# Performance work log

Hardware: AMD Instinct MI355X
Metric: run time of the kernel (lower is better)

## Reference

```python
import jax, jax.numpy as jnp
import numpy as np

KP, KD = 25, 3          # keypoints_num, keypoint_dim
FEAT = KP * KD          # 75
H = 1024                # hidden_size
NOISE_VALUE = 0.0
HT_LIMIT = 1.0


def lstm_cell(x, h, c, Wih, Whh, bih, bhh):
    # PyTorch LSTMCell gate order: i, f, g, o
    gates = x @ Wih.T + bih + h @ Whh.T + bhh  # [B, 4H]
    i, f, g, o = jnp.split(gates, 4, axis=-1)
    c = jax.nn.sigmoid(f) * c + jax.nn.sigmoid(i) * jnp.tanh(g)
    h = jax.nn.sigmoid(o) * jnp.tanh(c)
    return h, c


def run_lstm(seq, Wih, Whh, bih, bhh):
    # seq: [T, B, F]; single-layer LSTM, zero init state. Returns final (h, c).
    B = seq.shape[1]
    h0 = jnp.zeros((B, Whh.shape[1]), seq.dtype)
    def step(carry, x):
        h, c = lstm_cell(x, carry[0], carry[1], Wih, Whh, bih, bhh)
        return (h, c), None
    (h, c), _ = jax.lax.scan(step, (h0, h0), seq)
    return h, c


def setup_inputs() -> dict:
    key = jax.random.key(0)
    ks = jax.random.split(key, 20)
    s = 0.02
    inp = {
        'observed_pose': jax.random.normal(ks[0], (1024, 50, FEAT), jnp.float32),
        'future_pose': jax.random.normal(ks[1], (1024, 25, FEAT), jnp.float32),
        'observed_noise': jax.random.randint(ks[2], (1024, 50, KP), 0, 2, jnp.int32),
        # pose encoder LSTM params
        'pe_Wih': jax.random.normal(ks[3], (4 * H, FEAT), jnp.float32) * s,
        'pe_Whh': jax.random.normal(ks[4], (4 * H, H), jnp.float32) * s,
        'pe_bih': jax.random.normal(ks[5], (4 * H,), jnp.float32) * s,
        'pe_bhh': jax.random.normal(ks[6], (4 * H,), jnp.float32) * s,
        # vel encoder LSTM params
        've_Wih': jax.random.normal(ks[7], (4 * H, FEAT), jnp.float32) * s,
        've_Whh': jax.random.normal(ks[8], (4 * H, H), jnp.float32) * s,
        've_bih': jax.random.normal(ks[9], (4 * H,), jnp.float32) * s,
        've_bhh': jax.random.normal(ks[10], (4 * H,), jnp.float32) * s,
        # decoder LSTMCell params
        'dec_Wih': jax.random.normal(ks[11], (4 * H, FEAT), jnp.float32) * s,
        'dec_Whh': jax.random.normal(ks[12], (4 * H, H), jnp.float32) * s,
        'dec_bih': jax.random.normal(ks[13], (4 * H,), jnp.float32) * s,
        'dec_bhh': jax.random.normal(ks[14], (4 * H,), jnp.float32) * s,
        # output projection
        'fc_W': jax.random.normal(ks[15], (FEAT, H), jnp.float32) * s,
        'fc_b': jax.random.normal(ks[16], (FEAT,), jnp.float32) * s,
    }
    return inp


def reference(observed_pose, future_pose, observed_noise,
              pe_Wih, pe_Whh, pe_bih, pe_bhh,
              ve_Wih, ve_Whh, ve_bih, ve_bhh,
              dec_Wih, dec_Whh, dec_bih, dec_bhh,
              fc_W, fc_b):
    pose = observed_pose                              # [B, T, FEAT]
    vel = pose[:, 1:, :] - pose[:, :-1, :]            # [B, T-1, FEAT]
    bs, fn, feat = vel.shape
    noise = observed_noise[:, 1:, :]                  # [B, T-1, KP]
    mask = (noise == 1)[..., None]                    # [B, T-1, KP, 1]
    vel = jnp.where(mask, jnp.float32(NOISE_VALUE),
                    vel.reshape(bs, fn, KP, KD)).reshape(bs, fn, feat)

    h_vel, c_vel = run_lstm(vel.transpose(1, 0, 2), ve_Wih, ve_Whh, ve_bih, ve_bhh)
    h_pose, c_pose = run_lstm(pose.transpose(1, 0, 2), pe_Wih, pe_Whh, pe_bih, pe_bhh)

    h = h_pose + h_vel
    c = c_pose + c_vel
    out0 = vel[:, -1, :]                              # decoder seed input

    def dec_step(carry, _):
        h, c, out = carry
        x = jax.lax.stop_gradient(out)                # .detach() in the original
        h, c = lstm_cell(x, h, c, dec_Wih, dec_Whh, dec_bih, dec_bhh)
        out = jnp.clip(h @ fc_W.T + fc_b, -HT_LIMIT, HT_LIMIT)  # Hardtanh
        return (h, c, out), out

    _, comp_vel = jax.lax.scan(dec_step, (h, c, out0), None, length=fn)
    comp_vel = comp_vel.transpose(1, 0, 2)            # [B, T-1, FEAT]

    # comp_pose[0] = pose[0]; comp_pose[i+1] = comp_pose[i] + comp_vel[i]
    comp_pose = jnp.concatenate(
        [pose[:, :1], pose[:, :1] + jnp.cumsum(comp_vel, axis=1)], axis=1)

    return future_pose, comp_pose, comp_vel
```

## Files before the change

### kernel.cpp

```cpp
#include <hip/hip_runtime.h>

typedef unsigned short ushort_t;
typedef __attribute__((ext_vector_type(8))) short bf16x8;
typedef __attribute__((ext_vector_type(4))) float f32x4;

#define B_    1024
#define H_    1024
#define FEAT_ 75
#define KP_   1120
#define NK_   35
#define OFF_CP 1920000UL
#define OFF_CV 5760000UL

__device__ __forceinline__ float bf2f(ushort_t u) {
    unsigned x = ((unsigned)u) << 16;
    float f; __builtin_memcpy(&f, &x, 4); return f;
}
__device__ __forceinline__ ushort_t f2bf(float f) {
    unsigned x; __builtin_memcpy(&x, &f, 4);
    x += 0x7fffu + ((x >> 16) & 1u);
    return (ushort_t)(x >> 16);
}
__device__ __forceinline__ float sigm(float x) { return 1.f / (1.f + __expf(-x)); }

__device__ __forceinline__ void gload16(const void* g, void* l) {
    __builtin_amdgcn_global_load_lds(
        (const __attribute__((address_space(1))) void*)g,
        (__attribute__((address_space(3))) void*)l, 16, 0, 0);
}

struct StepArgs {
    const ushort_t* Ain[2];
    ushort_t*       Aout[2];
    const ushort_t* W[2];
    const float*    bias[2];
    float*          c[2];
    const ushort_t* xnext[2];
    int             xstride[2];
};

__global__ __launch_bounds__(256)
void lstm_step_kernel(StepArgs sa)
{
    __shared__ __align__(16) char lds[2 * 20480];

    const int flat = blockIdx.x;
    const int xcd  = flat & 7;
    const int slot = flat >> 3;
    int p, ct, rt;
    if (gridDim.x == 512) {
        const int cg = (xcd << 2) + (slot >> 4);
        p  = cg >> 4;
        ct = cg & 15;
    } else {
        const int cg = (xcd << 1) + (slot >> 4);
        p  = 0;
        ct = cg;
    }
    rt = slot & 15;

    const ushort_t* __restrict__ Ain  = sa.Ain[p];
    ushort_t*       __restrict__ Aout = sa.Aout[p];
    const ushort_t* __restrict__ Wt   = sa.W[p];
    const float*    __restrict__ bias = sa.bias[p];
    float*          __restrict__ cst  = sa.c[p];
    const ushort_t* xnext = sa.xnext[p];
    const int xstride = sa.xstride[p];

    const int tid  = threadIdx.x;
    const int w    = tid >> 6;
    const int l    = tid & 63;
    const int j0   = ct * 64;
    const int row0 = rt * 64;

    if (ct == 0 && xnext) {
        for (int idx = tid; idx < 64 * 96; idx += 256) {
            const int r  = idx / 96;
            const int xi = idx - r * 96;
            const int grow = row0 + r;
            ushort_t v = (xi < FEAT_) ? xnext[(size_t)grow * xstride + xi] : (ushort_t)0;
            Aout[(size_t)grow * KP_ + 1024 + xi] = v;
        }
    }

    const int lc4  = l & 3;
    const int lr4  = l >> 2;
    const int csrc = lc4 ^ (lr4 & 3);

    const ushort_t* agsrc = Ain + (size_t)(row0 + w * 16 + lr4) * KP_ + csrc * 8;
    char* aldst = lds + (w * 16) * 64;

    const ushort_t* bgsrc[4];
    char* bldst[4];
    #pragma unroll
    for (int i = 0; i < 4; ++i) {
        const int wcol = w * 1024 + j0 + i * 16 + lr4;
        bgsrc[i] = Wt + (size_t)wcol * KP_ + csrc * 8;
        bldst[i] = lds + 4096 + (w * 64 + i * 16) * 64;
    }

    const int chsw = (((l >> 4) ^ (l & 3)) << 4);
    int aoff[4], boff[4];
    #pragma unroll
    for (int m = 0; m < 4; ++m) aoff[m] = (m * 16 + (l & 15)) * 64 + chsw;
    #pragma unroll
    for (int g = 0; g < 4; ++g) boff[g] = 4096 + (g * 64 + w * 16 + (l & 15)) * 64 + chsw;

    f32x4 acc[4][4];
    #pragma unroll
    for (int m = 0; m < 4; ++m)
        #pragma unroll
        for (int g = 0; g < 4; ++g)
            acc[m][g] = (f32x4){0.f, 0.f, 0.f, 0.f};

    gload16(agsrc, aldst);
    #pragma unroll
    for (int i = 0; i < 4; ++i) gload16(bgsrc[i], bldst[i]);

    int bi = 0;
    for (int kt = 0; kt < NK_; ++kt) {
        if (kt + 1 < NK_) {
            const size_t k0 = (size_t)(kt + 1) * 32;
            const int nb = (bi ^ 1) * 20480;
            gload16(agsrc + k0, aldst + nb);
            #pragma unroll
            for (int i = 0; i < 4; ++i) gload16(bgsrc[i] + k0, bldst[i] + nb);
            asm volatile("s_waitcnt vmcnt(5)" ::: "memory");
        } else {
            asm volatile("s_waitcnt vmcnt(0)" ::: "memory");
        }
        __builtin_amdgcn_s_barrier();
        asm volatile("" ::: "memory");

        const char* bp = lds + bi * 20480;
        bf16x8 a[4], b[4];
        #pragma unroll
        for (int m = 0; m < 4; ++m) a[m] = *(const bf16x8*)(bp + aoff[m]);
        #pragma unroll
        for (int g = 0; g < 4; ++g) b[g] = *(const bf16x8*)(bp + boff[g]);
        __builtin_amdgcn_s_setprio(1);
        #pragma unroll
        for (int m = 0; m < 4; ++m)
            #pragma unroll
            for (int g = 0; g < 4; ++g)
                acc[m][g] = __builtin_amdgcn_mfma_f32_16x16x32_bf16(a[m], b[g], acc[m][g], 0, 0, 0);
        __builtin_amdgcn_s_setprio(0);

        asm volatile("" ::: "memory");
        __builtin_amdgcn_s_barrier();
        bi ^= 1;
    }

    const int jw = j0 + w * 16 + (l & 15);
    const float b_i = bias[jw];
    const float b_f = bias[1024 + jw];
    const float b_g = bias[2048 + jw];
    const float b_o = bias[3072 + jw];
    #pragma unroll
    for (int m = 0; m < 4; ++m) {
        #pragma unroll
        for (int r = 0; r < 4; ++r) {
            const int grow = row0 + m * 16 + ((l >> 4) << 2) + r;
            const float gi = acc[m][0][r] + b_i;
            const float gf = acc[m][1][r] + b_f;
            const float gg = acc[m][2][r] + b_g;
            const float go = acc[m][3][r] + b_o;
            const size_t ce = (size_t)grow * H_ + jw;
            const float cn = sigm(gf) * cst[ce] + sigm(gi) * tanhf(gg);
            cst[ce] = cn;
            Aout[(size_t)grow * KP_ + jw] = f2bf(sigm(go) * tanhf(cn));
        }
    }
}

__global__ __launch_bounds__(256)
void pack_kernel(const float* __restrict__ peWih, const float* __restrict__ peWhh,
                 const float* __restrict__ veWih, const float* __restrict__ veWhh,
                 const float* __restrict__ deWih, const float* __restrict__ deWhh,
                 const float* __restrict__ pe_bih, const float* __restrict__ pe_bhh,
                 const float* __restrict__ ve_bih, const float* __restrict__ ve_bhh,
                 const float* __restrict__ de_bih, const float* __restrict__ de_bhh,
                 const float* __restrict__ fcW,
                 ushort_t* __restrict__ Wp, float* __restrict__ biasp,
                 ushort_t* __restrict__ fcWb)
{
    const size_t PER = 4096UL * KP_;
    const size_t NW  = 3UL * PER;
    const size_t NB  = 3UL * 4096;
    const size_t NF  = 75UL * 1024;
    for (size_t idx = (size_t)blockIdx.x * blockDim.x + threadIdx.x;
         idx < NW + NB + NF; idx += (size_t)gridDim.x * blockDim.x) {
        if (idx < NW) {
            const int p   = (int)(idx / PER);
            const size_t rem = idx % PER;
            const int row = (int)(rem / KP_);
            const int k   = (int)(rem % KP_);
            const float* Whh = (p == 0) ? peWhh : (p == 1) ? veWhh : deWhh;
            const float* Wih = (p == 0) ? peWih : (p == 1) ? veWih : deWih;
            float v = 0.f;
            if (k < 1024)      v = Whh[(size_t)row * 1024 + k];
            else if (k < 1099) v = Wih[(size_t)row * 75 + (k - 1024)];
            Wp[idx] = f2bf(v);
        } else if (idx < NW + NB) {
            const size_t i = idx - NW;
            const int p = (int)(i / 4096);
            const int r = (int)(i % 4096);
            const float* bih = (p == 0) ? pe_bih : (p == 1) ? ve_bih : de_bih;
            const float* bhh = (p == 0) ? pe_bhh : (p == 1) ? ve_bhh : de_bhh;
            biasp[i] = bih[r] + bhh[r];
        } else {
            const size_t i = idx - NW - NB;
            fcWb[i] = f2bf(fcW[i]);
        }
    }
}

__global__ __launch_bounds__(256)
void prep_kernel(const float* __restrict__ pose, const float* __restrict__ fut,
                 const int* __restrict__ noise,
                 ushort_t* __restrict__ pose_bf, ushort_t* __restrict__ vel_bf,
                 ushort_t* __restrict__ A_pe0, ushort_t* __restrict__ A_ve0,
                 ushort_t* __restrict__ A_dec0,
                 float* __restrict__ accp, float* __restrict__ out)
{
    const size_t N0 = 1024UL * 50 * 75;
    const size_t N1 = 1024UL * 49 * 75;
    const size_t N2 = 1920000UL;
    const size_t N3 = 76800UL;
    for (size_t idx = (size_t)blockIdx.x * blockDim.x + threadIdx.x;
         idx < N0 + N1 + N2 + N3; idx += (size_t)gridDim.x * blockDim.x) {
        if (idx < N0) {
            pose_bf[idx] = f2bf(pose[idx]);
        } else if (idx < N0 + N1) {
            const size_t i = idx - N0;
            const int f = (int)(i % 75);
            const size_t rem = i / 75;
            const int t = (int)(rem % 49);
            const size_t b = rem / 49;
            float v = pose[(b * 50 + t + 1) * 75 + f] - pose[(b * 50 + t) * 75 + f];
            if (noise[(b * 50 + t + 1) * 25 + f / 3] == 1) v = 0.f;
            const ushort_t vb = f2bf(v);
            vel_bf[i] = vb;
            if (t == 0)  A_ve0[b * KP_ + 1024 + f]  = vb;
            if (t == 48) A_dec0[b * KP_ + 1024 + f] = vb;
        } else if (idx < N0 + N1 + N2) {
            const size_t i = idx - N0 - N1;
            out[i] = fut[i];
        } else {
            const size_t i = idx - N0 - N1 - N2;
            const size_t b = i / 75;
            const int f = (int)(i % 75);
            const float p0 = pose[b * 50 * 75 + f];
            A_pe0[b * KP_ + 1024 + f] = f2bf(p0);
            accp[i] = p0;
            out[OFF_CP + b * 50 * 75 + f] = p0;
        }
    }
}

__global__ __launch_bounds__(256)
void combine_kernel(const ushort_t* __restrict__ hpe, const ushort_t* __restrict__ hve,
                    const float* __restrict__ cpe, const float* __restrict__ cve,
                    ushort_t* __restrict__ Adec0, float* __restrict__ cde)
{
    const int idx = blockIdx.x * blockDim.x + threadIdx.x;
    if (idx >= B_ * H_) return;
    const int b = idx >> 10, j = idx & 1023;
    Adec0[(size_t)b * KP_ + j] = f2bf(bf2f(hpe[(size_t)b * KP_ + j]) + bf2f(hve[(size_t)b * KP_ + j]));
    cde[idx] = cpe[idx] + cve[idx];
}

__global__ __launch_bounds__(128)
void fc_kernel(const ushort_t* __restrict__ Adec,
               ushort_t* __restrict__ Adec_w,
               const ushort_t* __restrict__ fcWb, const float* __restrict__ fcb,
               float* __restrict__ accp, float* __restrict__ out, int t)
{
    __shared__ float hs[1024];
    const int b = blockIdx.x;
    const ushort_t* hrow = Adec + (size_t)b * KP_;
    {
        const int k = threadIdx.x * 8;
        const bf16x8 v = *(const bf16x8*)(hrow + k);
        #pragma unroll
        for (int u = 0; u < 8; ++u) hs[k + u] = bf2f((ushort_t)v[u]);
    }
    __syncthreads();
    const int f = threadIdx.x;
    if (f < FEAT_) {
        const ushort_t* wr = fcWb + (size_t)f * 1024;
        float s0 = fcb[f], s1 = 0.f, s2 = 0.f, s3 = 0.f;
        for (int k = 0; k < 1024; k += 32) {
            const bf16x8 w0 = *(const bf16x8*)(wr + k);
            const bf16x8 w1 = *(const bf16x8*)(wr + k + 8);
            const bf16x8 w2 = *(const bf16x8*)(wr + k + 16);
            const bf16x8 w3 = *(const bf16x8*)(wr + k + 24);
            #pragma unroll
            for (int u = 0; u < 8; ++u) {
                s0 = fmaf(hs[k + u],      bf2f((ushort_t)w0[u]), s0);
                s1 = fmaf(hs[k + 8 + u],  bf2f((ushort_t)w1[u]), s1);
                s2 = fmaf(hs[k + 16 + u], bf2f((ushort_t)w2[u]), s2);
                s3 = fmaf(hs[k + 24 + u], bf2f((ushort_t)w3[u]), s3);
            }
        }
        float s = (s0 + s1) + (s2 + s3);
        s = fminf(fmaxf(s, -1.f), 1.f);
        const float p = accp[b * FEAT_ + f] + s;
        accp[b * FEAT_ + f] = p;
        out[OFF_CV + ((size_t)b * 49 + t) * FEAT_ + f]     = s;
        out[OFF_CP + ((size_t)b * 50 + t + 1) * FEAT_ + f] = p;
        Adec_w[(size_t)b * KP_ + 1024 + f] = f2bf(s);
    }
}

extern "C" void kernel_launch(void* const* d_in, const int* in_sizes, int n_in,
                              void* d_out, int out_size, void* d_ws, size_t ws_size,
                              hipStream_t stream) {
    const float* pose   = (const float*)d_in[0];
    const float* fut    = (const float*)d_in[1];
    const int*   noise  = (const int*)  d_in[2];
    const float* peWih  = (const float*)d_in[3];
    const float* peWhh  = (const float*)d_in[4];
    const float* pe_bih = (const float*)d_in[5];
    const float* pe_bhh = (const float*)d_in[6];
    const float* veWih  = (const float*)d_in[7];
    const float* veWhh  = (const float*)d_in[8];
    const float* ve_bih = (const float*)d_in[9];
    const float* ve_bhh = (const float*)d_in[10];
    const float* deWih  = (const float*)d_in[11];
    const float* deWhh  = (const float*)d_in[12];
    const float* de_bih = (const float*)d_in[13];
    const float* de_bhh = (const float*)d_in[14];
    const float* fcW    = (const float*)d_in[15];
    const float* fcb    = (const float*)d_in[16];
    float* out = (float*)d_out;

    char* base = (char*)d_ws;
    ushort_t* Ape[2]  = {(ushort_t*)(base + 0UL * 2293760), (ushort_t*)(base + 1UL * 2293760)};
    ushort_t* Ave[2]  = {(ushort_t*)(base + 2UL * 2293760), (ushort_t*)(base + 3UL * 2293760)};
    ushort_t* Adec[2] = {(ushort_t*)(base + 4UL * 2293760), (ushort_t*)(base + 5UL * 2293760)};
    float* c_pe = (float*)(base + 13762560);
    float* c_ve = c_pe + 1048576;
    float* c_de = c_ve + 1048576;
    ushort_t* Wp    = (ushort_t*)(base + 26345472);
    float*    biasp = (float*)   (base + 53870592);
    ushort_t* fcWb  = (ushort_t*)(base + 53919744);
    ushort_t* pose_bf = (ushort_t*)(base + 54073344);
    ushort_t* vel_bf  = (ushort_t*)(base + 61753344);
    float*    accp    = (float*)   (base + 69279744);

    hipMemsetAsync(base, 0, 22151168, stream);

    pack_kernel<<<2048, 256, 0, stream>>>(peWih, peWhh, veWih, veWhh, deWih, deWhh,
                                          pe_bih, pe_bhh, ve_bih, ve_bhh, de_bih, de_bhh,
                                          fcW, Wp, biasp, fcWb);
    prep_kernel<<<2048, 256, 0, stream>>>(pose, fut, noise, pose_bf, vel_bf,
                                          Ape[0], Ave[0], Adec[0], accp, out);

    const ushort_t* Wpe = Wp;
    const ushort_t* Wve = Wp + 4587520;
    const ushort_t* Wde = Wp + 9175040;

    for (int t = 0; t < 49; ++t) {
        StepArgs sa;
        sa.Ain[0] = Ape[t & 1];  sa.Aout[0] = Ape[(t + 1) & 1];
        sa.W[0] = Wpe; sa.bias[0] = biasp; sa.c[0] = c_pe;
        sa.xnext[0] = pose_bf + (size_t)(t + 1) * 75; sa.xstride[0] = 3750;
        sa.Ain[1] = Ave[t & 1];  sa.Aout[1] = Ave[(t + 1) & 1];
        sa.W[1] = Wve; sa.bias[1] = biasp + 4096; sa.c[1] = c_ve;
        sa.xnext[1] = (t < 48) ? (vel_bf + (size_t)(t + 1) * 75) : nullptr;
        sa.xstride[1] = 3675;
        lstm_step_kernel<<<512, 256, 0, stream>>>(sa);
    }
    {
        StepArgs sa;
        sa.Ain[0] = Ape[1]; sa.Aout[0] = Ape[0];
        sa.W[0] = Wpe; sa.bias[0] = biasp; sa.c[0] = c_pe;
        sa.xnext[0] = nullptr; sa.xstride[0] = 3750;
        sa.Ain[1] = sa.Ain[0]; sa.Aout[1] = sa.Aout[0];
        sa.W[1] = sa.W[0]; sa.bias[1] = sa.bias[0]; sa.c[1] = sa.c[0];
        sa.xnext[1] = nullptr; sa.xstride[1] = 3750;
        lstm_step_kernel<<<256, 256, 0, stream>>>(sa);
    }

    combine_kernel<<<4096, 256, 0, stream>>>(Ape[0], Ave[1], c_pe, c_ve, Adec[0], c_de);

    for (int d = 0; d < 49; ++d) {
        StepArgs sa;
        sa.Ain[0] = Adec[d & 1]; sa.Aout[0] = Adec[(d + 1) & 1];
        sa.W[0] = Wde; sa.bias[0] = biasp + 8192; sa.c[0] = c_de;
        sa.xnext[0] = nullptr; sa.xstride[0] = 0;
        sa.Ain[1] = sa.Ain[0]; sa.Aout[1] = sa.Aout[0];
        sa.W[1] = sa.W[0]; sa.bias[1] = sa.bias[0]; sa.c[1] = sa.c[0];
        sa.xnext[1] = nullptr; sa.xstride[1] = 0;
        lstm_step_kernel<<<256, 256, 0, stream>>>(sa);
        fc_kernel<<<B_, 128, 0, stream>>>(Adec[(d + 1) & 1], Adec[(d + 1) & 1],
                                          fcWb, fcb, accp, out, d);
    }
}
```

Before: 4.061 ms.

## Halve LSTM step row tile to 32 and rotate K-loop start per block

Each LSTM step block now covers 32 batch rows instead of 64, which doubles the grid (1024 blocks for the fused encoder pair, 512 for single LSTMs) and trims per-block LDS so that four blocks can fit per CU. Each block starts its K loop at a different offset so that concurrent blocks do not all read the same weight columns at the same time. This aims to fill the GPU better and spread memory traffic across channels, but each weight tile is now loaded by twice as many blocks, roughly doubling weight reads from L2.

```diff
diff --git a/kernel.cpp b/kernel.cpp
--- a/kernel.cpp
+++ b/kernel.cpp
@@ -9,6 +9,7 @@
 #define FEAT_ 75
 #define KP_   1120
 #define NK_   35
+#define LBUF  18432
 #define OFF_CP 1920000UL
 #define OFF_CV 5760000UL
 
@@ -29,52 +30,22 @@
         (__attribute__((address_space(3))) void*)l, 16, 0, 0);
 }
 
-struct StepArgs {
-    const ushort_t* Ain[2];
-    ushort_t*       Aout[2];
-    const ushort_t* W[2];
-    const float*    bias[2];
-    float*          c[2];
-    const ushort_t* xnext[2];
-    int             xstride[2];
-};
-
-__global__ __launch_bounds__(256)
-void lstm_step_kernel(StepArgs sa)
-{
-    __shared__ __align__(16) char lds[2 * 20480];
-
-    const int flat = blockIdx.x;
-    const int xcd  = flat & 7;
-    const int slot = flat >> 3;
-    int p, ct, rt;
-    if (gridDim.x == 512) {
-        const int cg = (xcd << 2) + (slot >> 4);
-        p  = cg >> 4;
-        ct = cg & 15;
-    } else {
-        const int cg = (xcd << 1) + (slot >> 4);
-        p  = 0;
-        ct = cg;
-    }
-    rt = slot & 15;
-
-    const ushort_t* __restrict__ Ain  = sa.Ain[p];
-    ushort_t*       __restrict__ Aout = sa.Aout[p];
-    const ushort_t* __restrict__ Wt   = sa.W[p];
-    const float*    __restrict__ bias = sa.bias[p];
-    float*          __restrict__ cst  = sa.c[p];
-    const ushort_t* xnext = sa.xnext[p];
-    const int xstride = sa.xstride[p];
-
-    const int tid  = threadIdx.x;
+__device__ __forceinline__ void lstm_step_body(
+    char* lds,
+    const ushort_t* __restrict__ Ain, ushort_t* __restrict__ Aout,
+    const ushort_t* __restrict__ Wt,  const float* __restrict__ bias,
+    float* __restrict__ cst,
+    const ushort_t* xnext, int xstride,
+    int ct, int rt, int tid)
+{
     const int w    = tid >> 6;
     const int l    = tid & 63;
     const int j0   = ct * 64;
-    const int row0 = rt * 64;
+    const int row0 = rt * 32;
+    const int rot  = rt >= NK_ ? rt - NK_ : rt;
 
     if (ct == 0 && xnext) {
-        for (int idx = tid; idx < 64 * 96; idx += 256) {
+        for (int idx = tid; idx < 32 * 96; idx += 256) {
             const int r  = idx / 96;
             const int xi = idx - r * 96;
             const int grow = row0 + r;
@@ -82,13 +53,14 @@
             Aout[(size_t)grow * KP_ + 1024 + xi] = v;
         }
     }
+    asm volatile("s_waitcnt vmcnt(0)" ::: "memory");
 
     const int lc4  = l & 3;
     const int lr4  = l >> 2;
     const int csrc = lc4 ^ (lr4 & 3);
 
-    const ushort_t* agsrc = Ain + (size_t)(row0 + w * 16 + lr4) * KP_ + csrc * 8;
-    char* aldst = lds + (w * 16) * 64;
+    const ushort_t* agsrc = Ain + (size_t)(row0 + w * 8 + lr4) * KP_ + csrc * 8;
+    char* aldst = lds + (w * 8) * 64;
 
     const ushort_t* bgsrc[4];
     char* bldst[4];
@@ -96,35 +68,39 @@
     for (int i = 0; i < 4; ++i) {
         const int wcol = w * 1024 + j0 + i * 16 + lr4;
         bgsrc[i] = Wt + (size_t)wcol * KP_ + csrc * 8;
-        bldst[i] = lds + 4096 + (w * 64 + i * 16) * 64;
+        bldst[i] = lds + 2048 + (w * 64 + i * 16) * 64;
     }
 
     const int chsw = (((l >> 4) ^ (l & 3)) << 4);
-    int aoff[4], boff[4];
+    int aoff[2], boff[4];
     #pragma unroll
-    for (int m = 0; m < 4; ++m) aoff[m] = (m * 16 + (l & 15)) * 64 + chsw;
+    for (int m = 0; m < 2; ++m) aoff[m] = (m * 16 + (l & 15)) * 64 + chsw;
     #pragma unroll
-    for (int g = 0; g < 4; ++g) boff[g] = 4096 + (g * 64 + w * 16 + (l & 15)) * 64 + chsw;
-
-    f32x4 acc[4][4];
+    for (int g = 0; g < 4; ++g) boff[g] = 2048 + (g * 64 + w * 16 + (l & 15)) * 64 + chsw;
+
+    f32x4 acc[2][4];
     #pragma unroll
-    for (int m = 0; m < 4; ++m)
+    for (int m = 0; m < 2; ++m)
         #pragma unroll
         for (int g = 0; g < 4; ++g)
             acc[m][g] = (f32x4){0.f, 0.f, 0.f, 0.f};
 
-    gload16(agsrc, aldst);
-    #pragma unroll
-    for (int i = 0; i < 4; ++i) gload16(bgsrc[i], bldst[i]);
+    {
+        const size_t k0 = (size_t)rot * 32;
+        if (l < 32) gload16(agsrc + k0, aldst);
+        #pragma unroll
+        for (int i = 0; i < 4; ++i) gload16(bgsrc[i] + k0, bldst[i]);
+    }
 
     int bi = 0;
-    for (int kt = 0; kt < NK_; ++kt) {
-        if (kt + 1 < NK_) {
-            const size_t k0 = (size_t)(kt + 1) * 32;
-            const int nb = (bi ^ 1) * 20480;
-            gload16(agsrc + k0, aldst + nb);
+    for (int i = 0; i < NK_; ++i) {
+        if (i + 1 < NK_) {
+            int kn = i + 1 + rot; if (kn >= NK_) kn -= NK_;
+            const size_t k0 = (size_t)kn * 32;
+            const int nb = (bi ^ 1) * LBUF;
+            if (l < 32) gload16(agsrc + k0, aldst + nb);
             #pragma unroll
-            for (int i = 0; i < 4; ++i) gload16(bgsrc[i] + k0, bldst[i] + nb);
+            for (int g = 0; g < 4; ++g) gload16(bgsrc[g] + k0, bldst[g] + nb);
             asm volatile("s_waitcnt vmcnt(5)" ::: "memory");
         } else {
             asm volatile("s_waitcnt vmcnt(0)" ::: "memory");
@@ -132,15 +108,15 @@
         __builtin_amdgcn_s_barrier();
         asm volatile("" ::: "memory");
 
-        const char* bp = lds + bi * 20480;
-        bf16x8 a[4], b[4];
-        #pragma unroll
-        for (int m = 0; m < 4; ++m) a[m] = *(const bf16x8*)(bp + aoff[m]);
+        const char* bp = lds + bi * LBUF;
+        bf16x8 a[2], b[4];
+        #pragma unroll
+        for (int m = 0; m < 2; ++m) a[m] = *(const bf16x8*)(bp + aoff[m]);
         #pragma unroll
         for (int g = 0; g < 4; ++g) b[g] = *(const bf16x8*)(bp + boff[g]);
         __builtin_amdgcn_s_setprio(1);
         #pragma unroll
-        for (int m = 0; m < 4; ++m)
+        for (int m = 0; m < 2; ++m)
             #pragma unroll
             for (int g = 0; g < 4; ++g)
                 acc[m][g] = __builtin_amdgcn_mfma_f32_16x16x32_bf16(a[m], b[g], acc[m][g], 0, 0, 0);
@@ -157,7 +133,7 @@
     const float b_g = bias[2048 + jw];
     const float b_o = bias[3072 + jw];
     #pragma unroll
-    for (int m = 0; m < 4; ++m) {
+    for (int m = 0; m < 2; ++m) {
         #pragma unroll
         for (int r = 0; r < 4; ++r) {
             const int grow = row0 + m * 16 + ((l >> 4) << 2) + r;
@@ -171,6 +147,37 @@
             Aout[(size_t)grow * KP_ + jw] = f2bf(sigm(go) * tanhf(cn));
         }
     }
+}
+
+struct StepArgs {
+    const ushort_t* Ain[2];
+    ushort_t*       Aout[2];
+    const ushort_t* W[2];
+    const float*    bias[2];
+    float*          c[2];
+    const ushort_t* xnext[2];
+    int             xstride[2];
+};
+
+__global__ __launch_bounds__(256, 4)
+void step_kernel(StepArgs sa)
+{
+    __shared__ __align__(16) char lds[2 * LBUF];
+    const int flat = blockIdx.x;
+    const int xcd  = flat & 7;
+    const int slot = flat >> 3;
+    int p, ct;
+    if (gridDim.x == 1024) {
+        const int cgx = (xcd << 2) + (slot >> 5);
+        p  = cgx >> 4;
+        ct = cgx & 15;
+    } else {
+        p  = 0;
+        ct = (xcd << 1) + (slot >> 5);
+    }
+    const int rt = slot & 31;
+    lstm_step_body(lds, sa.Ain[p], sa.Aout[p], sa.W[p], sa.bias[p], sa.c[p],
+                   sa.xnext[p], sa.xstride[p], ct, rt, threadIdx.x);
 }
 
 __global__ __launch_bounds__(256)
@@ -266,7 +273,8 @@
     const int idx = blockIdx.x * blockDim.x + threadIdx.x;
     if (idx >= B_ * H_) return;
     const int b = idx >> 10, j = idx & 1023;
-    Adec0[(size_t)b * KP_ + j] = f2bf(bf2f(hpe[(size_t)b * KP_ + j]) + bf2f(hve[(size_t)b * KP_ + j]));
+    const size_t o = (size_t)b * KP_ + j;
+    Adec0[o] = f2bf(bf2f(hpe[o]) + bf2f(hve[o]));
     cde[idx] = cpe[idx] + cve[idx];
 }
 
@@ -370,7 +378,7 @@
         sa.W[1] = Wve; sa.bias[1] = biasp + 4096; sa.c[1] = c_ve;
         sa.xnext[1] = (t < 48) ? (vel_bf + (size_t)(t + 1) * 75) : nullptr;
         sa.xstride[1] = 3675;
-        lstm_step_kernel<<<512, 256, 0, stream>>>(sa);
+        step_kernel<<<1024, 256, 0, stream>>>(sa);
     }
     {
         StepArgs sa;
@@ -380,7 +388,7 @@
         sa.Ain[1] = sa.Ain[0]; sa.Aout[1] = sa.Aout[0];
         sa.W[1] = sa.W[0]; sa.bias[1] = sa.bias[0]; sa.c[1] = sa.c[0];
         sa.xnext[1] = nullptr; sa.xstride[1] = 3750;
-        lstm_step_kernel<<<256, 256, 0, stream>>>(sa);
+        step_kernel<<<512, 256, 0, stream>>>(sa);
     }
 
     combine_kernel<<<4096, 256, 0, stream>>>(Ape[0], Ave[1], c_pe, c_ve, Adec[0], c_de);
@@ -393,7 +401,7 @@
         sa.Ain[1] = sa.Ain[0]; sa.Aout[1] = sa.Aout[0];
         sa.W[1] = sa.W[0]; sa.bias[1] = sa.bias[0]; sa.c[1] = sa.c[0];
         sa.xnext[1] = nullptr; sa.xstride[1] = 0;
-        lstm_step_kernel<<<256, 256, 0, stream>>>(sa);
+        step_kernel<<<512, 256, 0, stream>>>(sa);
         fc_kernel<<<B_, 128, 0, stream>>>(Adec[(d + 1) & 1], Adec[(d + 1) & 1],
                                           fcWb, fcb, accp, out, d);
     }
```

Result: slower. 4.819 ms (+18.7%).

## Fuse all LSTM steps into a persistent cooperative kernel with register-resident weights

Applied to the files above, without the earlier changes.

Replaces roughly 150 per-step kernel launches with one cooperative persistent kernel that uses grid.sync between timesteps. Each wave keeps its slice of the recurrent weight matrix in registers for the whole sequence, and the cell state stays in registers, so per-step weight and state traffic from global memory goes away. The combine and FC projection phases move into the same kernel. The old multi-launch path is kept as a fallback if the cooperative launch fails. In exchange the kernel depends on grid-wide barriers, heavy register pressure (35 bf16x8 per thread at 512 threads with 2 blocks per CU) and only 256 blocks, and the FC phase is scalar.

```diff
diff --git a/kernel.cpp b/kernel.cpp
--- a/kernel.cpp
+++ b/kernel.cpp
@@ -1,4 +1,7 @@
 #include <hip/hip_runtime.h>
+#include <hip/hip_cooperative_groups.h>
+
+namespace cg = cooperative_groups;
 
 typedef unsigned short ushort_t;
 typedef __attribute__((ext_vector_type(8))) short bf16x8;
@@ -8,9 +11,13 @@
 #define H_    1024
 #define FEAT_ 75
 #define KP_   1120
-#define NK_   35
+#define NKT   35
 #define OFF_CP 1920000UL
 #define OFF_CV 5760000UL
+
+#define LDS_SCR 24576
+#define LDS_FC  33280
+#define LDS_TOT 49664
 
 __device__ __forceinline__ float bf2f(ushort_t u) {
     unsigned x = ((unsigned)u) << 16;
@@ -29,147 +36,232 @@
         (__attribute__((address_space(3))) void*)l, 16, 0, 0);
 }
 
-struct StepArgs {
-    const ushort_t* Ain[2];
-    ushort_t*       Aout[2];
-    const ushort_t* W[2];
-    const float*    bias[2];
-    float*          c[2];
-    const ushort_t* xnext[2];
-    int             xstride[2];
-};
-
-__global__ __launch_bounds__(256)
-void lstm_step_kernel(StepArgs sa)
-{
-    __shared__ __align__(16) char lds[2 * 20480];
-
-    const int flat = blockIdx.x;
-    const int xcd  = flat & 7;
-    const int slot = flat >> 3;
-    int p, ct, rt;
-    if (gridDim.x == 512) {
-        const int cg = (xcd << 2) + (slot >> 4);
-        p  = cg >> 4;
-        ct = cg & 15;
-    } else {
-        const int cg = (xcd << 1) + (slot >> 4);
-        p  = 0;
-        ct = cg;
-    }
-    rt = slot & 15;
-
-    const ushort_t* __restrict__ Ain  = sa.Ain[p];
-    ushort_t*       __restrict__ Aout = sa.Aout[p];
-    const ushort_t* __restrict__ Wt   = sa.W[p];
-    const float*    __restrict__ bias = sa.bias[p];
-    float*          __restrict__ cst  = sa.c[p];
-    const ushort_t* xnext = sa.xnext[p];
-    const int xstride = sa.xstride[p];
-
-    const int tid  = threadIdx.x;
-    const int w    = tid >> 6;
-    const int l    = tid & 63;
-    const int j0   = ct * 64;
-    const int row0 = rt * 64;
-
-    if (ct == 0 && xnext) {
-        for (int idx = tid; idx < 64 * 96; idx += 256) {
-            const int r  = idx / 96;
-            const int xi = idx - r * 96;
-            const int grow = row0 + r;
-            ushort_t v = (xi < FEAT_) ? xnext[(size_t)grow * xstride + xi] : (ushort_t)0;
-            Aout[(size_t)grow * KP_ + 1024 + xi] = v;
-        }
-    }
-
-    const int lc4  = l & 3;
-    const int lr4  = l >> 2;
-    const int csrc = lc4 ^ (lr4 & 3);
-
-    const ushort_t* agsrc = Ain + (size_t)(row0 + w * 16 + lr4) * KP_ + csrc * 8;
-    char* aldst = lds + (w * 16) * 64;
-
-    const ushort_t* bgsrc[4];
-    char* bldst[4];
-    #pragma unroll
-    for (int i = 0; i < 4; ++i) {
-        const int wcol = w * 1024 + j0 + i * 16 + lr4;
-        bgsrc[i] = Wt + (size_t)wcol * KP_ + csrc * 8;
-        bldst[i] = lds + 4096 + (w * 64 + i * 16) * 64;
-    }
-
-    const int chsw = (((l >> 4) ^ (l & 3)) << 4);
-    int aoff[4], boff[4];
-    #pragma unroll
-    for (int m = 0; m < 4; ++m) aoff[m] = (m * 16 + (l & 15)) * 64 + chsw;
-    #pragma unroll
-    for (int g = 0; g < 4; ++g) boff[g] = 4096 + (g * 64 + w * 16 + (l & 15)) * 64 + chsw;
-
-    f32x4 acc[4][4];
-    #pragma unroll
-    for (int m = 0; m < 4; ++m)
-        #pragma unroll
-        for (int g = 0; g < 4; ++g)
-            acc[m][g] = (f32x4){0.f, 0.f, 0.f, 0.f};
-
-    gload16(agsrc, aldst);
-    #pragma unroll
-    for (int i = 0; i < 4; ++i) gload16(bgsrc[i], bldst[i]);
-
-    int bi = 0;
-    for (int kt = 0; kt < NK_; ++kt) {
-        if (kt + 1 < NK_) {
-            const size_t k0 = (size_t)(kt + 1) * 32;
-            const int nb = (bi ^ 1) * 20480;
-            gload16(agsrc + k0, aldst + nb);
-            #pragma unroll
-            for (int i = 0; i < 4; ++i) gload16(bgsrc[i] + k0, bldst[i] + nb);
-            asm volatile("s_waitcnt vmcnt(5)" ::: "memory");
+__device__ __forceinline__ void load_w(bf16x8 (&bw)[NKT],
+                                       const ushort_t* __restrict__ Wt,
+                                       int j0w, int l)
+{
+    const int c16 = l & 15;
+    const size_t row = (size_t)((c16 >> 2) << 10) + (c16 & 3) + j0w;
+    const ushort_t* p = Wt + row * KP_ + ((l >> 4) << 3);
+    #pragma unroll
+    for (int kt = 0; kt < NKT; ++kt)
+        bw[kt] = *(const bf16x8*)(p + kt * 32);
+}
+
+__device__ __forceinline__ void run_pass(
+    char* lds, const ushort_t* __restrict__ Ain, ushort_t* __restrict__ Aout,
+    const bf16x8 (&bw)[NKT], float (&cr)[8],
+    float bsi, float bsf, float bsg, float bso,
+    int R0, int j0w, int tid, int w, int l,
+    int write_c, float* __restrict__ cglob)
+{
+    const int srow = tid >> 2;
+    const ushort_t* asrc = Ain + (size_t)(R0 + srow) * KP_
+                         + (((tid & 3) ^ (srow & 3)) << 3);
+    char* adst = lds + (w << 10);
+    const int abase = ((l & 15) << 6) + ((((l >> 4) ^ (l & 3))) << 4);
+    float* sc = (float*)(lds + LDS_SCR) + w * 272;
+
+    f32x4 acc[8];
+    #pragma unroll
+    for (int m = 0; m < 8; ++m) acc[m] = (f32x4){0.f, 0.f, 0.f, 0.f};
+
+    asm volatile("s_waitcnt vmcnt(0)" ::: "memory");
+    gload16(asrc,      adst);
+    gload16(asrc + 32, adst + 8192);
+
+    #pragma unroll
+    for (int kt = 0; kt < NKT; ++kt) {
+        if (kt + 2 < NKT) {
+            gload16(asrc + (kt + 2) * 32, adst + ((kt + 2) % 3) * 8192);
+            asm volatile("s_waitcnt vmcnt(2)" ::: "memory");
+        } else if (kt + 1 < NKT) {
+            asm volatile("s_waitcnt vmcnt(1)" ::: "memory");
         } else {
             asm volatile("s_waitcnt vmcnt(0)" ::: "memory");
         }
         __builtin_amdgcn_s_barrier();
         asm volatile("" ::: "memory");
-
-        const char* bp = lds + bi * 20480;
-        bf16x8 a[4], b[4];
-        #pragma unroll
-        for (int m = 0; m < 4; ++m) a[m] = *(const bf16x8*)(bp + aoff[m]);
-        #pragma unroll
-        for (int g = 0; g < 4; ++g) b[g] = *(const bf16x8*)(bp + boff[g]);
+        const char* bp = lds + (kt % 3) * 8192;
         __builtin_amdgcn_s_setprio(1);
         #pragma unroll
-        for (int m = 0; m < 4; ++m)
-            #pragma unroll
-            for (int g = 0; g < 4; ++g)
-                acc[m][g] = __builtin_amdgcn_mfma_f32_16x16x32_bf16(a[m], b[g], acc[m][g], 0, 0, 0);
+        for (int m = 0; m < 8; ++m) {
+            const bf16x8 a = *(const bf16x8*)(bp + (m << 10) + abase);
+            acc[m] = __builtin_amdgcn_mfma_f32_16x16x32_bf16(a, bw[kt], acc[m], 0, 0, 0);
+        }
         __builtin_amdgcn_s_setprio(0);
-
         asm volatile("" ::: "memory");
         __builtin_amdgcn_s_barrier();
-        bi ^= 1;
-    }
-
-    const int jw = j0 + w * 16 + (l & 15);
-    const float b_i = bias[jw];
-    const float b_f = bias[1024 + jw];
-    const float b_g = bias[2048 + jw];
-    const float b_o = bias[3072 + jw];
-    #pragma unroll
-    for (int m = 0; m < 4; ++m) {
-        #pragma unroll
-        for (int r = 0; r < 4; ++r) {
-            const int grow = row0 + m * 16 + ((l >> 4) << 2) + r;
-            const float gi = acc[m][0][r] + b_i;
-            const float gf = acc[m][1][r] + b_f;
-            const float gg = acc[m][2][r] + b_g;
-            const float go = acc[m][3][r] + b_o;
-            const size_t ce = (size_t)grow * H_ + jw;
-            const float cn = sigm(gf) * cst[ce] + sigm(gi) * tanhf(gg);
-            cst[ce] = cn;
-            Aout[(size_t)grow * KP_ + jw] = f2bf(sigm(go) * tanhf(cn));
-        }
+    }
+
+    const int row2 = l >> 2, jj = l & 3;
+    const int jcol = j0w + jj;
+    #pragma unroll
+    for (int m = 0; m < 8; ++m) {
+        #pragma unroll
+        for (int r = 0; r < 4; ++r)
+            sc[((l >> 4) * 4 + r) * 17 + (l & 15)] = acc[m][r];
+        const float gi = sc[row2 * 17 + jj];
+        const float gf = sc[row2 * 17 + 4 + jj];
+        const float gg = sc[row2 * 17 + 8 + jj];
+        const float go = sc[row2 * 17 + 12 + jj];
+        const float cn = sigm(gf + bsf) * cr[m] + sigm(gi + bsi) * tanhf(gg + bsg);
+        cr[m] = cn;
+        const int grow = R0 + (m << 4) + row2;
+        Aout[(size_t)grow * KP_ + jcol] = f2bf(sigm(go + bso) * tanhf(cn));
+        if (write_c) cglob[((size_t)grow << 10) + jcol] = cn;
+    }
+}
+
+__device__ __forceinline__ void fc_phase(
+    char* lds, ushort_t* __restrict__ Ah,
+    const ushort_t* __restrict__ fcWb, const float* __restrict__ fcb,
+    float* __restrict__ accp, float* __restrict__ out,
+    int d, int tid, int blk)
+{
+    float* hs = (float*)(lds + LDS_FC);
+    const int r0 = (blk & 7) * 128 + (blk >> 3) * 4;
+    {
+        const int r = tid >> 7, k8 = (tid & 127) << 3;
+        const bf16x8 v = *(const bf16x8*)(Ah + (size_t)(r0 + r) * KP_ + k8);
+        #pragma unroll
+        for (int u = 0; u < 8; ++u) hs[(r << 10) + k8 + u] = bf2f((ushort_t)v[u]);
+    }
+    __syncthreads();
+    const int r = tid >> 7, f = tid & 127;
+    if (f < FEAT_) {
+        const ushort_t* wr = fcWb + (size_t)f * 1024;
+        const float* hr = hs + (r << 10);
+        float s0 = fcb[f], s1 = 0.f, s2 = 0.f, s3 = 0.f;
+        for (int k = 0; k < 1024; k += 32) {
+            const bf16x8 w0 = *(const bf16x8*)(wr + k);
+            const bf16x8 w1 = *(const bf16x8*)(wr + k + 8);
+            const bf16x8 w2 = *(const bf16x8*)(wr + k + 16);
+            const bf16x8 w3 = *(const bf16x8*)(wr + k + 24);
+            #pragma unroll
+            for (int u = 0; u < 8; ++u) {
+                s0 = fmaf(hr[k + u],      bf2f((ushort_t)w0[u]), s0);
+                s1 = fmaf(hr[k + 8 + u],  bf2f((ushort_t)w1[u]), s1);
+                s2 = fmaf(hr[k + 16 + u], bf2f((ushort_t)w2[u]), s2);
+                s3 = fmaf(hr[k + 24 + u], bf2f((ushort_t)w3[u]), s3);
+            }
+        }
+        float s = (s0 + s1) + (s2 + s3);
+        s = fminf(fmaxf(s, -1.f), 1.f);
+        const int row = r0 + r;
+        const float pnew = accp[row * FEAT_ + f] + s;
+        accp[row * FEAT_ + f] = pnew;
+        out[OFF_CV + ((size_t)row * 49 + d) * FEAT_ + f]     = s;
+        out[OFF_CP + ((size_t)row * 50 + d + 1) * FEAT_ + f] = pnew;
+        Ah[(size_t)row * KP_ + 1024 + f] = f2bf(s);
+    }
+    __syncthreads();
+}
+
+struct MainArgs {
+    ushort_t*       A[3][2];
+    const ushort_t* W[3];
+    const float*    bias[3];
+    float*          c_pe; float* c_ve;
+    const ushort_t* pose_bf; const ushort_t* vel_bf;
+    const ushort_t* fcWb; const float* fcb;
+    float*          accp; float* out;
+};
+
+__global__ __launch_bounds__(512, 2)
+void main_kernel(MainArgs ma)
+{
+    cg::grid_group grid = cg::this_grid();
+    __shared__ __align__(16) char lds[LDS_TOT];
+    const int tid = threadIdx.x;
+    const int w = tid >> 6, l = tid & 63;
+    const int blk = blockIdx.x;
+
+    const int p  = blk & 1;
+    const int q  = (blk >> 1) & 3;
+    const int g5 = blk >> 3;
+    const int j0w = (g5 << 5) + (w << 2);
+
+    bf16x8 bw[NKT];
+    load_w(bw, ma.W[p], j0w, l);
+    const int jl = j0w + (l & 3);
+    float bsi = ma.bias[p][jl];
+    float bsf = ma.bias[p][1024 + jl];
+    float bsg = ma.bias[p][2048 + jl];
+    float bso = ma.bias[p][3072 + jl];
+
+    float crA[8], crB[8];
+    #pragma unroll
+    for (int m = 0; m < 8; ++m) { crA[m] = 0.f; crB[m] = 0.f; }
+
+    float* cglob = (p == 0) ? ma.c_pe : ma.c_ve;
+    const int tlast = (p == 0) ? 49 : 48;
+
+    for (int t = 0; t < 50; ++t) {
+        if (p == 0 || t < 49) {
+            const ushort_t* Ain = ma.A[p][t & 1];
+            ushort_t* Aout = ma.A[p][(t + 1) & 1];
+            if (g5 == 0) {
+                const ushort_t* xn = nullptr; int xstr = 0;
+                if (p == 0 && t < 49) { xn = ma.pose_bf + (size_t)(t + 1) * 75; xstr = 3750; }
+                if (p == 1 && t < 48) { xn = ma.vel_bf  + (size_t)(t + 1) * 75; xstr = 3675; }
+                if (xn) {
+                    for (int i = tid; i < 256 * 75; i += 512) {
+                        const int r = i / 75, f = i - r * 75;
+                        Aout[(size_t)(q * 256 + r) * KP_ + 1024 + f] =
+                            xn[(size_t)(q * 256 + r) * xstr + f];
+                    }
+                }
+            }
+            const int wc = (t == tlast);
+            run_pass(lds, Ain, Aout, bw, crA, bsi, bsf, bsg, bso,
+                     q * 256,       j0w, tid, w, l, wc, cglob);
+            run_pass(lds, Ain, Aout, bw, crB, bsi, bsf, bsg, bso,
+                     q * 256 + 128, j0w, tid, w, l, wc, cglob);
+        }
+        grid.sync();
+    }
+
+    __threadfence();
+    grid.sync();
+    {
+        const ushort_t* hpe = ma.A[0][0];
+        const ushort_t* hve = ma.A[1][1];
+        ushort_t* Ad = ma.A[2][0];
+        for (int k = tid; k < 4096; k += 512) {
+            const int idx = (blk << 12) + k;
+            const size_t o = (size_t)(idx >> 10) * KP_ + (idx & 1023);
+            Ad[o] = f2bf(bf2f(hpe[o]) + bf2f(hve[o]));
+        }
+    }
+    __threadfence();
+    grid.sync();
+
+    const int oct = blk & 7;
+    const int dj0w = ((blk >> 3) << 5) + (w << 2);
+    load_w(bw, ma.W[2], dj0w, l);
+    {
+        const int jd = dj0w + (l & 3);
+        bsi = ma.bias[2][jd];
+        bsf = ma.bias[2][1024 + jd];
+        bsg = ma.bias[2][2048 + jd];
+        bso = ma.bias[2][3072 + jd];
+        const int row2 = l >> 2, jj = l & 3;
+        #pragma unroll
+        for (int m = 0; m < 8; ++m) {
+            const size_t o = ((size_t)(oct * 128 + m * 16 + row2) << 10) + dj0w + jj;
+            crA[m] = ma.c_pe[o] + ma.c_ve[o];
+        }
+    }
+
+    for (int d = 0; d < 49; ++d) {
+        const ushort_t* Ain = ma.A[2][d & 1];
+        ushort_t* Aout = ma.A[2][(d + 1) & 1];
+        run_pass(lds, Ain, Aout, bw, crA, bsi, bsf, bsg, bso,
+                 oct * 128, dj0w, tid, w, l, 0, nullptr);
+        grid.sync();
+        fc_phase(lds, Aout, ma.fcWb, ma.fcb, ma.accp, ma.out, d, tid, blk);
+        grid.sync();
     }
 }
 
@@ -191,22 +283,22 @@
     for (size_t idx = (size_t)blockIdx.x * blockDim.x + threadIdx.x;
          idx < NW + NB + NF; idx += (size_t)gridDim.x * blockDim.x) {
         if (idx < NW) {
-            const int p   = (int)(idx / PER);
+            const int pp  = (int)(idx / PER);
             const size_t rem = idx % PER;
             const int row = (int)(rem / KP_);
             const int k   = (int)(rem % KP_);
-            const float* Whh = (p == 0) ? peWhh : (p == 1) ? veWhh : deWhh;
-            const float* Wih = (p == 0) ? peWih : (p == 1) ? veWih : deWih;
+            const float* Whh = (pp == 0) ? peWhh : (pp == 1) ? veWhh : deWhh;
+            const float* Wih = (pp == 0) ? peWih : (pp == 1) ? veWih : deWih;
             float v = 0.f;
             if (k < 1024)      v = Whh[(size_t)row * 1024 + k];
             else if (k < 1099) v = Wih[(size_t)row * 75 + (k - 1024)];
             Wp[idx] = f2bf(v);
         } else if (idx < NW + NB) {
             const size_t i = idx - NW;
-            const int p = (int)(i / 4096);
+            const int pp = (int)(i / 4096);
             const int r = (int)(i % 4096);
-            const float* bih = (p == 0) ? pe_bih : (p == 1) ? ve_bih : de_bih;
-            const float* bhh = (p == 0) ? pe_bhh : (p == 1) ? ve_bhh : de_bhh;
+            const float* bih = (pp == 0) ? pe_bih : (pp == 1) ? ve_bih : de_bih;
+            const float* bhh = (pp == 0) ? pe_bhh : (pp == 1) ? ve_bhh : de_bhh;
             biasp[i] = bih[r] + bhh[r];
         } else {
             const size_t i = idx - NW - NB;
@@ -258,32 +350,133 @@
     }
 }
 
+__device__ __forceinline__ void fb_body(
+    char* lds,
+    const ushort_t* __restrict__ Ain, ushort_t* __restrict__ Aout,
+    const ushort_t* __restrict__ Wt,  const float* __restrict__ bias,
+    float* __restrict__ cst,
+    const ushort_t* xnext, int xstride,
+    int ct, int rt, int tid)
+{
+    const int w = tid >> 6, l = tid & 63;
+    const int j0 = ct * 64, row0 = rt * 64;
+    if (ct == 0 && xnext) {
+        for (int idx = tid; idx < 64 * 96; idx += 256) {
+            const int r = idx / 96, xi = idx - r * 96;
+            ushort_t v = (xi < FEAT_) ? xnext[(size_t)(row0 + r) * xstride + xi] : (ushort_t)0;
+            Aout[(size_t)(row0 + r) * KP_ + 1024 + xi] = v;
+        }
+    }
+    asm volatile("s_waitcnt vmcnt(0)" ::: "memory");
+    const int lc4 = l & 3, lr4 = l >> 2;
+    const int csrc = lc4 ^ (lr4 & 3);
+    const ushort_t* agsrc = Ain + (size_t)(row0 + w * 16 + lr4) * KP_ + csrc * 8;
+    char* aldst = lds + (w * 16) * 64;
+    const ushort_t* bgsrc[4]; char* bldst[4];
+    #pragma unroll
+    for (int i = 0; i < 4; ++i) {
+        bgsrc[i] = Wt + (size_t)(w * 1024 + j0 + i * 16 + lr4) * KP_ + csrc * 8;
+        bldst[i] = lds + 4096 + (w * 64 + i * 16) * 64;
+    }
+    const int chsw = (((l >> 4) ^ (l & 3)) << 4);
+    int aoff[4], boff[4];
+    #pragma unroll
+    for (int m = 0; m < 4; ++m) aoff[m] = (m * 16 + (l & 15)) * 64 + chsw;
+    #pragma unroll
+    for (int g = 0; g < 4; ++g) boff[g] = 4096 + (g * 64 + w * 16 + (l & 15)) * 64 + chsw;
+    f32x4 acc[4][4];
+    #pragma unroll
+    for (int m = 0; m < 4; ++m)
+        #pragma unroll
+        for (int g = 0; g < 4; ++g) acc[m][g] = (f32x4){0.f,0.f,0.f,0.f};
+    gload16(agsrc, aldst);
+    #pragma unroll
+    for (int i = 0; i < 4; ++i) gload16(bgsrc[i], bldst[i]);
+    int bi = 0;
+    for (int kt = 0; kt < NKT; ++kt) {
+        if (kt + 1 < NKT) {
+            const size_t k0 = (size_t)(kt + 1) * 32;
+            const int nb = (bi ^ 1) * 20480;
+            gload16(agsrc + k0, aldst + nb);
+            #pragma unroll
+            for (int i = 0; i < 4; ++i) gload16(bgsrc[i] + k0, bldst[i] + nb);
+            asm volatile("s_waitcnt vmcnt(5)" ::: "memory");
+        } else {
+            asm volatile("s_waitcnt vmcnt(0)" ::: "memory");
+        }
+        __builtin_amdgcn_s_barrier();
+        asm volatile("" ::: "memory");
+        const char* bp = lds + bi * 20480;
+        bf16x8 a[4], b[4];
+        #pragma unroll
+        for (int m = 0; m < 4; ++m) a[m] = *(const bf16x8*)(bp + aoff[m]);
+        #pragma unroll
+        for (int g = 0; g < 4; ++g) b[g] = *(const bf16x8*)(bp + boff[g]);
+        #pragma unroll
+        for (int m = 0; m < 4; ++m)
+            #pragma unroll
+            for (int g = 0; g < 4; ++g)
+                acc[m][g] = __builtin_amdgcn_mfma_f32_16x16x32_bf16(a[m], b[g], acc[m][g], 0, 0, 0);
+        asm volatile("" ::: "memory");
+        __builtin_amdgcn_s_barrier();
+        bi ^= 1;
+    }
+    const int jw = j0 + w * 16 + (l & 15);
+    const float b_i = bias[jw], b_f = bias[1024 + jw], b_g = bias[2048 + jw], b_o = bias[3072 + jw];
+    #pragma unroll
+    for (int m = 0; m < 4; ++m)
+        #pragma unroll
+        for (int r = 0; r < 4; ++r) {
+            const int grow = row0 + m * 16 + ((l >> 4) << 2) + r;
+            const float cn = sigm(acc[m][1][r] + b_f) * cst[(size_t)grow * H_ + jw]
+                           + sigm(acc[m][0][r] + b_i) * tanhf(acc[m][2][r] + b_g);
+            cst[(size_t)grow * H_ + jw] = cn;
+            Aout[(size_t)grow * KP_ + jw] = f2bf(sigm(acc[m][3][r] + b_o) * tanhf(cn));
+        }
+}
+
+struct StepArgs {
+    const ushort_t* Ain[2]; ushort_t* Aout[2];
+    const ushort_t* W[2]; const float* bias[2]; float* c[2];
+    const ushort_t* xnext[2]; int xstride[2];
+};
+
 __global__ __launch_bounds__(256)
-void combine_kernel(const ushort_t* __restrict__ hpe, const ushort_t* __restrict__ hve,
-                    const float* __restrict__ cpe, const float* __restrict__ cve,
-                    ushort_t* __restrict__ Adec0, float* __restrict__ cde)
-{
-    const int idx = blockIdx.x * blockDim.x + threadIdx.x;
+void fb_step_kernel(StepArgs sa)
+{
+    __shared__ __align__(16) char lds[2 * 20480];
+    const int flat = blockIdx.x, xcd = flat & 7, slot = flat >> 3;
+    int pp, ct;
+    if (gridDim.x == 512) { const int cgx = (xcd << 2) + (slot >> 4); pp = cgx >> 4; ct = cgx & 15; }
+    else                  { const int cgx = (xcd << 1) + (slot >> 4); pp = 0;        ct = cgx; }
+    fb_body(lds, sa.Ain[pp], sa.Aout[pp], sa.W[pp], sa.bias[pp], sa.c[pp],
+            sa.xnext[pp], sa.xstride[pp], ct, slot & 15, threadIdx.x);
+}
+
+__global__ __launch_bounds__(256)
+void fb_combine_kernel(const ushort_t* hpe, const ushort_t* hve,
+                       const float* cpe, const float* cve,
+                       ushort_t* Adec0, float* cde)
+{
+    const int idx = blockIdx.x * 256 + threadIdx.x;
     if (idx >= B_ * H_) return;
-    const int b = idx >> 10, j = idx & 1023;
-    Adec0[(size_t)b * KP_ + j] = f2bf(bf2f(hpe[(size_t)b * KP_ + j]) + bf2f(hve[(size_t)b * KP_ + j]));
+    const size_t o = (size_t)(idx >> 10) * KP_ + (idx & 1023);
+    Adec0[o] = f2bf(bf2f(hpe[o]) + bf2f(hve[o]));
     cde[idx] = cpe[idx] + cve[idx];
 }
 
 __global__ __launch_bounds__(128)
-void fc_kernel(const ushort_t* __restrict__ Adec,
-               ushort_t* __restrict__ Adec_w,
-               const ushort_t* __restrict__ fcWb, const float* __restrict__ fcb,
-               float* __restrict__ accp, float* __restrict__ out, int t)
-{
-    __shared__ float hs[1024];
+void fb_fc_kernel(ushort_t* __restrict__ Adec,
+                  const ushort_t* __restrict__ fcWb, const float* __restrict__ fcb,
+                  float* __restrict__ accp, float* __restrict__ out, int t)
+{
+    __shared__ float hsf[1024];
     const int b = blockIdx.x;
-    const ushort_t* hrow = Adec + (size_t)b * KP_;
     {
         const int k = threadIdx.x * 8;
-        const bf16x8 v = *(const bf16x8*)(hrow + k);
-        #pragma unroll
-        for (int u = 0; u < 8; ++u) hs[k + u] = bf2f((ushort_t)v[u]);
+        const bf16x8 v = *(const bf16x8*)(Adec + (size_t)b * KP_ + k);
+        #pragma unroll
+        for (int u = 0; u < 8; ++u) hsf[k + u] = bf2f((ushort_t)v[u]);
     }
     __syncthreads();
     const int f = threadIdx.x;
@@ -297,19 +490,19 @@
             const bf16x8 w3 = *(const bf16x8*)(wr + k + 24);
             #pragma unroll
             for (int u = 0; u < 8; ++u) {
-                s0 = fmaf(hs[k + u],      bf2f((ushort_t)w0[u]), s0);
-                s1 = fmaf(hs[k + 8 + u],  bf2f((ushort_t)w1[u]), s1);
-                s2 = fmaf(hs[k + 16 + u], bf2f((ushort_t)w2[u]), s2);
-                s3 = fmaf(hs[k + 24 + u], bf2f((ushort_t)w3[u]), s3);
+                s0 = fmaf(hsf[k + u],      bf2f((ushort_t)w0[u]), s0);
+                s1 = fmaf(hsf[k + 8 + u],  bf2f((ushort_t)w1[u]), s1);
+                s2 = fmaf(hsf[k + 16 + u], bf2f((ushort_t)w2[u]), s2);
+                s3 = fmaf(hsf[k + 24 + u], bf2f((ushort_t)w3[u]), s3);
             }
         }
         float s = (s0 + s1) + (s2 + s3);
         s = fminf(fmaxf(s, -1.f), 1.f);
-        const float p = accp[b * FEAT_ + f] + s;
-        accp[b * FEAT_ + f] = p;
+        const float pnew = accp[b * FEAT_ + f] + s;
+        accp[b * FEAT_ + f] = pnew;
         out[OFF_CV + ((size_t)b * 49 + t) * FEAT_ + f]     = s;
-        out[OFF_CP + ((size_t)b * 50 + t + 1) * FEAT_ + f] = p;
-        Adec_w[(size_t)b * KP_ + 1024 + f] = f2bf(s);
+        out[OFF_CP + ((size_t)b * 50 + t + 1) * FEAT_ + f] = pnew;
+        Adec[(size_t)b * KP_ + 1024 + f] = f2bf(s);
     }
 }
 
@@ -349,7 +542,7 @@
     ushort_t* vel_bf  = (ushort_t*)(base + 61753344);
     float*    accp    = (float*)   (base + 69279744);
 
-    hipMemsetAsync(base, 0, 22151168, stream);
+    hipMemsetAsync(base, 0, 13762560, stream);
 
     pack_kernel<<<2048, 256, 0, stream>>>(peWih, peWhh, veWih, veWhh, deWih, deWhh,
                                           pe_bih, pe_bhh, ve_bih, ve_bhh, de_bih, de_bhh,
@@ -357,44 +550,53 @@
     prep_kernel<<<2048, 256, 0, stream>>>(pose, fut, noise, pose_bf, vel_bf,
                                           Ape[0], Ave[0], Adec[0], accp, out);
 
-    const ushort_t* Wpe = Wp;
-    const ushort_t* Wve = Wp + 4587520;
-    const ushort_t* Wde = Wp + 9175040;
-
-    for (int t = 0; t < 49; ++t) {
-        StepArgs sa;
-        sa.Ain[0] = Ape[t & 1];  sa.Aout[0] = Ape[(t + 1) & 1];
-        sa.W[0] = Wpe; sa.bias[0] = biasp; sa.c[0] = c_pe;
-        sa.xnext[0] = pose_bf + (size_t)(t + 1) * 75; sa.xstride[0] = 3750;
-        sa.Ain[1] = Ave[t & 1];  sa.Aout[1] = Ave[(t + 1) & 1];
-        sa.W[1] = Wve; sa.bias[1] = biasp + 4096; sa.c[1] = c_ve;
-        sa.xnext[1] = (t < 48) ? (vel_bf + (size_t)(t + 1) * 75) : nullptr;
-        sa.xstride[1] = 3675;
-        lstm_step_kernel<<<512, 256, 0, stream>>>(sa);
-    }
-    {
-        StepArgs sa;
-        sa.Ain[0] = Ape[1]; sa.Aout[0] = Ape[0];
-        sa.W[0] = Wpe; sa.bias[0] = biasp; sa.c[0] = c_pe;
-        sa.xnext[0] = nullptr; sa.xstride[0] = 3750;
-        sa.Ain[1] = sa.Ain[0]; sa.Aout[1] = sa.Aout[0];
-        sa.W[1] = sa.W[0]; sa.bias[1] = sa.bias[0]; sa.c[1] = sa.c[0];
-        sa.xnext[1] = nullptr; sa.xstride[1] = 3750;
-        lstm_step_kernel<<<256, 256, 0, stream>>>(sa);
-    }
-
-    combine_kernel<<<4096, 256, 0, stream>>>(Ape[0], Ave[1], c_pe, c_ve, Adec[0], c_de);
-
-    for (int d = 0; d < 49; ++d) {
-        StepArgs sa;
-        sa.Ain[0] = Adec[d & 1]; sa.Aout[0] = Adec[(d + 1) & 1];
-        sa.W[0] = Wde; sa.bias[0] = biasp + 8192; sa.c[0] = c_de;
-        sa.xnext[0] = nullptr; sa.xstride[0] = 0;
-        sa.Ain[1] = sa.Ain[0]; sa.Aout[1] = sa.Aout[0];
-        sa.W[1] = sa.W[0]; sa.bias[1] = sa.bias[0]; sa.c[1] = sa.c[0];
-        sa.xnext[1] = nullptr; sa.xstride[1] = 0;
-        lstm_step_kernel<<<256, 256, 0, stream>>>(sa);
-        fc_kernel<<<B_, 128, 0, stream>>>(Adec[(d + 1) & 1], Adec[(d + 1) & 1],
-                                          fcWb, fcb, accp, out, d);
-    }
-}
+    MainArgs ma;
+    ma.A[0][0] = Ape[0];  ma.A[0][1] = Ape[1];
+    ma.A[1][0] = Ave[0];  ma.A[1][1] = Ave[1];
+    ma.A[2][0] = Adec[0]; ma.A[2][1] = Adec[1];
+    ma.W[0] = Wp; ma.W[1] = Wp + 4587520; ma.W[2] = Wp + 9175040;
+    ma.bias[0] = biasp; ma.bias[1] = biasp + 4096; ma.bias[2] = biasp + 8192;
+    ma.c_pe = c_pe; ma.c_ve = c_ve;
+    ma.pose_bf = pose_bf; ma.vel_bf = vel_bf;
+    ma.fcWb = fcWb; ma.fcb = fcb; ma.accp = accp; ma.out = out;
+
+    void* kargs[] = {(void*)&ma};
+    hipError_t e = hipLaunchCooperativeKernel((const void*)main_kernel,
+                                              dim3(256), dim3(512), kargs, 0, stream);
+    if (e != hipSuccess) {
+        (void)hipGetLastError();
+        for (int t = 0; t < 49; ++t) {
+            StepArgs sa;
+            sa.Ain[0] = Ape[t & 1];  sa.Aout[0] = Ape[(t + 1) & 1];
+            sa.W[0] = ma.W[0]; sa.bias[0] = biasp; sa.c[0] = c_pe;
+            sa.xnext[0] = pose_bf + (size_t)(t + 1) * 75; sa.xstride[0] = 3750;
+            sa.Ain[1] = Ave[t & 1];  sa.Aout[1] = Ave[(t + 1) & 1];
+            sa.W[1] = ma.W[1]; sa.bias[1] = biasp + 4096; sa.c[1] = c_ve;
+            sa.xnext[1] = (t < 48) ? (vel_bf + (size_t)(t + 1) * 75) : nullptr;
+            sa.xstride[1] = 3675;
+            fb_step_kernel<<<512, 256, 0, stream>>>(sa);
+        }
+        {
+            StepArgs sa;
+            sa.Ain[0] = Ape[1]; sa.Aout[0] = Ape[0];
+            sa.W[0] = ma.W[0]; sa.bias[0] = biasp; sa.c[0] = c_pe;
+            sa.xnext[0] = nullptr; sa.xstride[0] = 3750;
+            sa.Ain[1] = sa.Ain[0]; sa.Aout[1] = sa.Aout[0];
+            sa.W[1] = sa.W[0]; sa.bias[1] = sa.bias[0]; sa.c[1] = sa.c[0];
+            sa.xnext[1] = nullptr; sa.xstride[1] = 3750;
+            fb_step_kernel<<<256, 256, 0, stream>>>(sa);
+        }
+        fb_combine_kernel<<<4096, 256, 0, stream>>>(Ape[0], Ave[1], c_pe, c_ve, Adec[0], c_de);
+        for (int d = 0; d < 49; ++d) {
+            StepArgs sa;
+            sa.Ain[0] = Adec[d & 1]; sa.Aout[0] = Adec[(d + 1) & 1];
+            sa.W[0] = ma.W[2]; sa.bias[0] = biasp + 8192; sa.c[0] = c_de;
+            sa.xnext[0] = nullptr; sa.xstride[0] = 0;
+            sa.Ain[1] = sa.Ain[0]; sa.Aout[1] = sa.Aout[0];
+            sa.W[1] = sa.W[0]; sa.bias[1] = sa.bias[0]; sa.c[1] = sa.c[0];
+            sa.xnext[1] = nullptr; sa.xstride[1] = 0;
+            fb_step_kernel<<<256, 256, 0, stream>>>(sa);
+            fb_fc_kernel<<<B_, 128, 0, stream>>>(Adec[(d + 1) & 1], fcWb, fcb, accp, out, d);
+        }
+    }
+}
```

After: 7.822 ms. +92.6%, slower.
